# Kernel optimization log

Measured on AMD Instinct MI355X. Metric: run time of the kernel, lower is better.

The kernel has to match this reference:

```python
import jax, jax.numpy as jnp
import numpy as np

B, N, E = 16, 50000, 1600000  # batch, num_nodes (excl. ground), num_edges


def setup_inputs() -> dict:
    key = jax.random.key(0)
    k1, k2, k3, k4 = jax.random.split(key, 4)
    x = jax.random.normal(k1, (B, N), dtype=jnp.float32)
    # node indices in [0, N]; index 0 is the ground node prepended in forward
    src_node = jax.random.randint(k2, (E,), 0, N + 1)
    des_node = jax.random.randint(k3, (E,), 0, N + 1)
    # per-edge device params (a, w, b), gauss init std=0.01 per _init_model_param
    param = jax.random.normal(k4, (3, E), dtype=jnp.float32) * 0.01
    t = jnp.zeros((1,), dtype=jnp.float32)
    return {"t": t, "x": x, "param": param, "src_node": src_node, "des_node": des_node}


def _edge_model(param, v_s, v_d):
    # per-edge nonlinear device current: i_e = a_e * tanh(w_e*(v_s - v_d) + b_e)
    a, w, b = param[0], param[1], param[2]
    return a * jnp.tanh(w * (v_s - v_d) + b)  # (B, E)


def reference(t, x, param, src_node, des_node):
    # prepend ground node (voltage 0) -> aux_v: (B, N+1)
    aux_v = jnp.concatenate([jnp.zeros_like(x[..., :1]), x], axis=-1)
    v_s = aux_v[:, src_node]  # gather (B, E)
    v_d = aux_v[:, des_node]  # gather (B, E)
    state_i = _edge_model(param, v_s, v_d)  # (B, E)
    # KCL: current leaves src, enters des; scatter_add along node axis
    res = jnp.zeros_like(aux_v)
    res = res.at[:, src_node].add(-state_i)
    res = res.at[:, des_node].add(state_i)
    return res[:, 1:]  # drop ground node
```

## Files before the change

kernel.cpp:

```cpp
#include <hip/hip_runtime.h>

#define BATCH 16
#define PS 49
#define NPART 1024
#define SB 256
#define TPB 1024
#define LDSCAP 3840

#define TWO_LOG2E 2.8853900817779268f

__global__ __launch_bounds__(TPB)
void hist1(const int* __restrict__ src, const int* __restrict__ des,
           const float* __restrict__ x, float* __restrict__ auxT,
           unsigned* __restrict__ blockHist, int E, int n) {
    __shared__ unsigned h[NPART];
    int tid = threadIdx.x;
    for (int i = tid; i < NPART; i += TPB) h[i] = 0;
    for (long idx = (long)blockIdx.x * TPB + tid; idx < (long)BATCH * n;
         idx += (long)gridDim.x * TPB) {
        int b = (int)(idx / n);
        int i = (int)(idx - (long)b * n);
        auxT[(size_t)(i + 1) * BATCH + b] = x[idx];
        if (idx < BATCH) auxT[idx] = 0.0f;
    }
    __syncthreads();
    long t = (long)blockIdx.x * TPB + tid;
    long stride = (long)gridDim.x * TPB * 4;
    for (long e0 = t * 4; e0 < E; e0 += stride) {
        int ne = (int)min((long)4, (long)E - e0);
        int ss[4], dd[4];
        if (ne == 4) {
            int4 sv = *(const int4*)(src + e0);
            int4 dv = *(const int4*)(des + e0);
            ss[0]=sv.x; ss[1]=sv.y; ss[2]=sv.z; ss[3]=sv.w;
            dd[0]=dv.x; dd[1]=dv.y; dd[2]=dv.z; dd[3]=dv.w;
        } else {
            for (int j = 0; j < ne; ++j) { ss[j] = src[e0+j]; dd[j] = des[e0+j]; }
        }
        for (int j = 0; j < ne; ++j) {
            atomicAdd(&h[ss[j] / PS], 1u);
            atomicAdd(&h[dd[j] / PS], 1u);
        }
    }
    __syncthreads();
    for (int i = tid; i < NPART; i += TPB)
        blockHist[(size_t)blockIdx.x * NPART + i] = h[i];
}

__global__ __launch_bounds__(TPB)
void totals_k(const unsigned* __restrict__ blockHist, unsigned* __restrict__ binTotal) {
    int tid = threadIdx.x;
    int bin = blockIdx.x * 64 + (tid >> 4);
    int j = tid & 15;
    unsigned s = 0;
    for (int r = j; r < SB; r += 16) s += blockHist[(size_t)r * NPART + bin];
#pragma unroll
    for (int m = 1; m < 16; m <<= 1) s += __shfl_xor(s, m, 64);
    if (j == 0) binTotal[bin] = s;
}

__global__ __launch_bounds__(TPB)
void scan_bins(const unsigned* __restrict__ binTotal, unsigned* __restrict__ partStart) {
    __shared__ unsigned wsum[16];
    int tid = threadIdx.x;
    int lane = tid & 63, wv = tid >> 6;
    unsigned v = binTotal[tid];
    unsigned inc = v;
    for (int off = 1; off < 64; off <<= 1) {
        unsigned t = __shfl_up(inc, off, 64);
        if (lane >= off) inc += t;
    }
    if (lane == 63) wsum[wv] = inc;
    __syncthreads();
    if (tid < 16) {
        unsigned w = wsum[tid], winc = w;
        for (int off = 1; off < 16; off <<= 1) {
            unsigned t = __shfl_up(winc, off, 64);
            if (tid >= off) winc += t;
        }
        wsum[tid] = winc - w;
    }
    __syncthreads();
    unsigned excl = (inc - v) + wsum[wv];
    partStart[tid] = excl;
    if (tid == TPB - 1) partStart[NPART] = excl + v;
}

__global__ __launch_bounds__(TPB)
void offs_k(unsigned* __restrict__ blockHist, const unsigned* __restrict__ partStart) {
    int tid = threadIdx.x;
    int binLocal = tid >> 4;
    int bin = blockIdx.x * 64 + binLocal;
    int j = tid & 15;
    const int per = SB / 16;
    unsigned ls = 0;
    for (int r = j * per; r < (j + 1) * per; ++r)
        ls += blockHist[(size_t)r * NPART + bin];
    int waveBase = (binLocal & 3) * 16;
    unsigned excl = 0;
    for (int k = 0; k < 16; ++k) {
        unsigned v = __shfl(ls, waveBase + k, 64);
        if (k < j) excl += v;
    }
    unsigned run = partStart[bin] + excl;
    for (int r = j * per; r < (j + 1) * per; ++r) {
        unsigned tmp = blockHist[(size_t)r * NPART + bin];
        blockHist[(size_t)r * NPART + bin] = run;
        run += tmp;
    }
}

__global__ __launch_bounds__(TPB)
void scatter1(const int* __restrict__ src, const int* __restrict__ des,
              const float* __restrict__ param, const unsigned* __restrict__ offsets,
              uint4* __restrict__ bins, int E) {
    __shared__ unsigned offs[NPART];
    int tid = threadIdx.x;
    for (int i = tid; i < NPART; i += TPB)
        offs[i] = offsets[(size_t)blockIdx.x * NPART + i];
    __syncthreads();
    long t = (long)blockIdx.x * TPB + tid;
    long stride = (long)gridDim.x * TPB * 4;
    for (long e0 = t * 4; e0 < E; e0 += stride) {
        int ne = (int)min((long)4, (long)E - e0);
        int ss[4], dd[4];
        float aa[4], ww[4], cc[4];
        if (ne == 4) {
            int4 sv = *(const int4*)(src + e0);
            int4 dv = *(const int4*)(des + e0);
            float4 av = *(const float4*)(param + e0);
            float4 wv = *(const float4*)(param + E + e0);
            float4 cv = *(const float4*)(param + 2 * (size_t)E + e0);
            ss[0]=sv.x; ss[1]=sv.y; ss[2]=sv.z; ss[3]=sv.w;
            dd[0]=dv.x; dd[1]=dv.y; dd[2]=dv.z; dd[3]=dv.w;
            aa[0]=av.x; aa[1]=av.y; aa[2]=av.z; aa[3]=av.w;
            ww[0]=wv.x; ww[1]=wv.y; ww[2]=wv.z; ww[3]=wv.w;
            cc[0]=cv.x; cc[1]=cv.y; cc[2]=cv.z; cc[3]=cv.w;
        } else {
            for (int j = 0; j < ne; ++j) {
                ss[j] = src[e0+j]; dd[j] = des[e0+j];
                aa[j] = param[e0+j]; ww[j] = param[E + e0 + j];
                cc[j] = param[2 * (size_t)E + e0 + j];
            }
        }
        for (int j = 0; j < ne; ++j) {
            int s = ss[j], d = dd[j];
            float wq = ww[j] * TWO_LOG2E, cq = cc[j] * TWO_LOG2E;
            unsigned slot = atomicAdd(&offs[s / PS], 1u);
            bins[slot] = make_uint4((unsigned)s | ((unsigned)d << 16),
                                    __float_as_uint(-aa[j]), __float_as_uint(wq),
                                    __float_as_uint(cq));
            unsigned slot2 = atomicAdd(&offs[d / PS], 1u);
            bins[slot2] = make_uint4((unsigned)d | ((unsigned)s << 16),
                                     __float_as_uint(aa[j]), __float_as_uint(-wq),
                                     __float_as_uint(cq));
        }
    }
}

static __device__ __forceinline__ float edge_eval(float a, float a2, float wq, float cq,
                                                  float dv) {
    float ez = __builtin_amdgcn_exp2f(__builtin_fmaf(wq, dv, cq));
    float r = __builtin_amdgcn_rcpf(ez + 1.0f);
    return __builtin_fmaf(-a2, r, a);
}

__global__ __launch_bounds__(TPB)
void sort_accumulate(const uint4* __restrict__ bins, const unsigned* __restrict__ partStart,
                     const float* __restrict__ auxT, float* __restrict__ out, int n) {
    extern __shared__ uint4 srec[];
    unsigned* bump = (unsigned*)(srec + LDSCAP);
    unsigned* ns   = bump + PS;
    int p = blockIdx.x;
    int tid = threadIdx.x;
    unsigned lo = partStart[p], hi = partStart[p + 1];
    unsigned cl = min(hi - lo, (unsigned)LDSCAP);
    int base = p * PS;

    for (int i = tid; i < PS; i += TPB) bump[i] = 0;
    __syncthreads();
    const unsigned* keys = (const unsigned*)bins;
    for (unsigned k = tid; k < cl; k += TPB) {
        unsigned o = keys[(size_t)(lo + k) * 4] & 0xFFFFu;
        atomicAdd(&bump[o - (unsigned)base], 1u);
    }
    __syncthreads();
    if (tid == 0) {
        unsigned run = 0;
        for (int i = 0; i < PS; ++i) {
            unsigned c = bump[i];
            ns[i] = run;
            bump[i] = run;
            run += c;
        }
        ns[PS] = run;
    }
    __syncthreads();
    for (unsigned k = tid; k < cl; k += TPB) {
        uint4 rec = bins[lo + k];
        unsigned slot = atomicAdd(&bump[(rec.x & 0xFFFFu) - (unsigned)base], 1u);
        srec[slot] = rec;
    }
    __syncthreads();
    int lane = tid & 63;
    int wv = tid >> 6;
    int ri = lane >> 2, lj = lane & 3;
    const float4* aux4 = (const float4*)auxT;
    for (int nl = wv; nl < PS; nl += TPB / 64) {
        int node = base + nl;
        if (node == 0 || node > n) continue;
        unsigned l2 = ns[nl], h2 = ns[nl + 1];
        float4 vo = aux4[(size_t)node * 4 + lj];
        float ax = 0.0f, ay = 0.0f, az = 0.0f, as_ = 0.0f;
        for (unsigned kk = l2; kk < h2; kk += 16) {
            unsigned k = kk + (unsigned)ri;
            uint4 rec;
            if (k < h2) rec = srec[k];
            else { rec.x = 0u; rec.y = 0u; rec.z = 0u; rec.w = 0u; }
            unsigned rem = rec.x >> 16;
            float4 vr = aux4[(size_t)rem * 4 + lj];
            float a = __uint_as_float(rec.y);
            float a2 = a + a;
            float wq = __uint_as_float(rec.z);
            float cq = __uint_as_float(rec.w);
            ax  += edge_eval(a, a2, wq, cq, vo.x - vr.x);
            ay  += edge_eval(a, a2, wq, cq, vo.y - vr.y);
            az  += edge_eval(a, a2, wq, cq, vo.z - vr.z);
            as_ += edge_eval(a, a2, wq, cq, vo.w - vr.w);
        }
        for (unsigned kk = lo + cl; kk < hi; kk += 16) {
            unsigned k = kk + (unsigned)ri;
            uint4 rec;
            if (k < hi) rec = bins[k];
            else { rec.x = 0u; rec.y = 0u; rec.z = 0u; rec.w = 0u; }
            if ((int)(rec.x & 0xFFFFu) != node) rec.y = 0u;
            unsigned rem = rec.x >> 16;
            float4 vr = aux4[(size_t)rem * 4 + lj];
            float a = __uint_as_float(rec.y);
            float a2 = a + a;
            float wq = __uint_as_float(rec.z);
            float cq = __uint_as_float(rec.w);
            ax  += edge_eval(a, a2, wq, cq, vo.x - vr.x);
            ay  += edge_eval(a, a2, wq, cq, vo.y - vr.y);
            az  += edge_eval(a, a2, wq, cq, vo.z - vr.z);
            as_ += edge_eval(a, a2, wq, cq, vo.w - vr.w);
        }
#pragma unroll
        for (int m = 4; m < 64; m <<= 1) {
            ax  += __shfl_xor(ax, m, 64);
            ay  += __shfl_xor(ay, m, 64);
            az  += __shfl_xor(az, m, 64);
            as_ += __shfl_xor(as_, m, 64);
        }
        if (lane < 4) {
            int j = node - 1;
            int b0 = lj * 4;
            out[(size_t)(b0 + 0) * n + j] = ax;
            out[(size_t)(b0 + 1) * n + j] = ay;
            out[(size_t)(b0 + 2) * n + j] = az;
            out[(size_t)(b0 + 3) * n + j] = as_;
        }
    }
}

__global__ void edge_direct(const float* __restrict__ param,
                            const int* __restrict__ src,
                            const int* __restrict__ des,
                            const float* __restrict__ x,
                            float* __restrict__ out, int E, int n) {
    int e = blockIdx.x * blockDim.x + threadIdx.x;
    if (e >= E) return;
    float a = param[e], w = param[E + e], c = param[2 * E + e];
    int s = src[e], d = des[e];
#pragma unroll
    for (int b = 0; b < BATCH; ++b) {
        float vs = s ? x[(size_t)b * n + (s - 1)] : 0.0f;
        float vd = d ? x[(size_t)b * n + (d - 1)] : 0.0f;
        float st = a * tanhf(w * (vs - vd) + c);
        if (s) atomicAdd(out + (size_t)b * n + (s - 1), -st);
        if (d) atomicAdd(out + (size_t)b * n + (d - 1), st);
    }
}

extern "C" void kernel_launch(void* const* d_in, const int* in_sizes, int n_in,
                              void* d_out, int out_size, void* d_ws, size_t ws_size,
                              hipStream_t stream) {
    const float* x     = (const float*)d_in[1];
    const float* param = (const float*)d_in[2];
    const int*   src   = (const int*)d_in[3];
    const int*   des   = (const int*)d_in[4];
    float* out = (float*)d_out;

    int E = in_sizes[3];
    int n = in_sizes[1] / BATCH;

    auto alignup = [](size_t v) { return (v + 255) & ~(size_t)255; };
    size_t auxBytes  = alignup((size_t)(n + 1) * BATCH * sizeof(float));
    size_t bhBytes   = alignup((size_t)SB * NPART * sizeof(unsigned));
    size_t psBytes   = alignup((size_t)(NPART + 1) * sizeof(unsigned));
    size_t btBytes   = alignup((size_t)NPART * sizeof(unsigned));
    size_t binBytes  = alignup((size_t)2 * E * sizeof(uint4));
    size_t need      = auxBytes + bhBytes + psBytes + btBytes + binBytes;

    size_t saLds = (size_t)LDSCAP * sizeof(uint4) + (2 * PS + 1 + 8) * sizeof(unsigned);

    if (ws_size >= need && (n + 1) <= NPART * PS && n <= 65534) {
        char* w = (char*)d_ws;
        float*    auxT      = (float*)w;     w += auxBytes;
        unsigned* blockHist = (unsigned*)w;  w += bhBytes;
        unsigned* partStart = (unsigned*)w;  w += psBytes;
        unsigned* binTotal  = (unsigned*)w;  w += btBytes;
        uint4*    bins      = (uint4*)w;

        hist1<<<SB, TPB, 0, stream>>>(src, des, x, auxT, blockHist, E, n);
        totals_k<<<NPART / 64, TPB, 0, stream>>>(blockHist, binTotal);
        scan_bins<<<1, TPB, 0, stream>>>(binTotal, partStart);
        offs_k<<<NPART / 64, TPB, 0, stream>>>(blockHist, partStart);
        scatter1<<<SB, TPB, 0, stream>>>(src, des, param, blockHist, bins, E);
        sort_accumulate<<<NPART, TPB, saLds, stream>>>(bins, partStart, auxT, out, n);
        return;
    }

    (void)hipMemsetAsync(out, 0, (size_t)out_size * sizeof(float), stream);
    edge_direct<<<(E + 255) / 256, 256, 0, stream>>>(param, src, des, x, out, E, n);
}
```

Measured before the change: 123.8 us.

## Tile x transpose through LDS, nontemporal bin stores, wave-scan prefix

The x→auxT transpose in hist1 now goes through a padded LDS tile, so both the global reads and the global writes are coalesced instead of strided scatter writes. The scatter1 bin writes use nontemporal stores to avoid polluting cache with streaming records. In sort_accumulate, the serial single-thread prefix sum over 49 bins becomes a wave-level shuffle scan. The tile loop adds two block barriers per tile and changes how blocks are assigned to the transpose work.

```diff
diff --git a/kernel.cpp b/kernel.cpp
--- a/kernel.cpp
+++ b/kernel.cpp
@@ -9,19 +9,28 @@
 
 #define TWO_LOG2E 2.8853900817779268f
 
+typedef unsigned int uint4v __attribute__((ext_vector_type(4)));
+
 __global__ __launch_bounds__(TPB)
 void hist1(const int* __restrict__ src, const int* __restrict__ des,
            const float* __restrict__ x, float* __restrict__ auxT,
            unsigned* __restrict__ blockHist, int E, int n) {
     __shared__ unsigned h[NPART];
+    __shared__ float tile[64 * 17];
     int tid = threadIdx.x;
     for (int i = tid; i < NPART; i += TPB) h[i] = 0;
-    for (long idx = (long)blockIdx.x * TPB + tid; idx < (long)BATCH * n;
-         idx += (long)gridDim.x * TPB) {
-        int b = (int)(idx / n);
-        int i = (int)(idx - (long)b * n);
-        auxT[(size_t)(i + 1) * BATCH + b] = x[idx];
-        if (idx < BATCH) auxT[idx] = 0.0f;
+    if (blockIdx.x == 0 && tid < BATCH) auxT[tid] = 0.0f;
+    int nTiles = (n + 63) / 64;
+    for (int t0 = blockIdx.x; t0 < nTiles; t0 += gridDim.x) {
+        int i0 = t0 * 64;
+        int b = tid >> 6, ii = tid & 63;
+        float v = (i0 + ii < n) ? x[(size_t)b * n + i0 + ii] : 0.0f;
+        __syncthreads();
+        tile[ii * 17 + b] = v;
+        __syncthreads();
+        int i2 = i0 + (tid >> 4);
+        if (i2 < n)
+            auxT[(size_t)(i2 + 1) * BATCH + (tid & 15)] = tile[(tid >> 4) * 17 + (tid & 15)];
     }
     __syncthreads();
     long t = (long)blockIdx.x * TPB + tid;
@@ -119,6 +128,7 @@
     for (int i = tid; i < NPART; i += TPB)
         offs[i] = offsets[(size_t)blockIdx.x * NPART + i];
     __syncthreads();
+    uint4v* binv = (uint4v*)bins;
     long t = (long)blockIdx.x * TPB + tid;
     long stride = (long)gridDim.x * TPB * 4;
     for (long e0 = t * 4; e0 < E; e0 += stride) {
@@ -147,13 +157,13 @@
             int s = ss[j], d = dd[j];
             float wq = ww[j] * TWO_LOG2E, cq = cc[j] * TWO_LOG2E;
             unsigned slot = atomicAdd(&offs[s / PS], 1u);
-            bins[slot] = make_uint4((unsigned)s | ((unsigned)d << 16),
-                                    __float_as_uint(-aa[j]), __float_as_uint(wq),
-                                    __float_as_uint(cq));
+            uint4v r1 = {(unsigned)s | ((unsigned)d << 16), __float_as_uint(-aa[j]),
+                         __float_as_uint(wq), __float_as_uint(cq)};
+            __builtin_nontemporal_store(r1, &binv[slot]);
             unsigned slot2 = atomicAdd(&offs[d / PS], 1u);
-            bins[slot2] = make_uint4((unsigned)d | ((unsigned)s << 16),
-                                     __float_as_uint(aa[j]), __float_as_uint(-wq),
-                                     __float_as_uint(cq));
+            uint4v r2 = {(unsigned)d | ((unsigned)s << 16), __float_as_uint(aa[j]),
+                         __float_as_uint(-wq), __float_as_uint(cq)};
+            __builtin_nontemporal_store(r2, &binv[slot2]);
         }
     }
 }
@@ -173,6 +183,8 @@
     unsigned* ns   = bump + PS;
     int p = blockIdx.x;
     int tid = threadIdx.x;
+    int lane = tid & 63;
+    int wv = tid >> 6;
     unsigned lo = partStart[p], hi = partStart[p + 1];
     unsigned cl = min(hi - lo, (unsigned)LDSCAP);
     int base = p * PS;
@@ -185,15 +197,16 @@
         atomicAdd(&bump[o - (unsigned)base], 1u);
     }
     __syncthreads();
-    if (tid == 0) {
-        unsigned run = 0;
-        for (int i = 0; i < PS; ++i) {
-            unsigned c = bump[i];
-            ns[i] = run;
-            bump[i] = run;
-            run += c;
-        }
-        ns[PS] = run;
+    if (wv == 0) {
+        unsigned v = (lane < PS) ? bump[lane] : 0u;
+        unsigned inc = v;
+        for (int off = 1; off < 64; off <<= 1) {
+            unsigned t = __shfl_up(inc, off, 64);
+            if (lane >= off) inc += t;
+        }
+        unsigned excl = inc - v;
+        if (lane < PS) { ns[lane] = excl; bump[lane] = excl; }
+        if (lane == PS - 1) ns[PS] = inc;
     }
     __syncthreads();
     for (unsigned k = tid; k < cl; k += TPB) {
@@ -202,8 +215,6 @@
         srec[slot] = rec;
     }
     __syncthreads();
-    int lane = tid & 63;
-    int wv = tid >> 6;
     int ri = lane >> 2, lj = lane & 3;
     const float4* aux4 = (const float4*)auxT;
     for (int nl = wv; nl < PS; nl += TPB / 64) {
```

Result: slower. 202.4 us (+63.5%).
